# Optimization experiments

Hardware: AMD Instinct MI355X
Metric: run time of the kernel (lower is better)

## Reference

```python
import jax, jax.numpy as jnp
import numpy as np

R, B, N, H = 10, 8, 8192, 8          # ROIs, patients, nodes/ROI-graph, inner hidden
K = N // 2                            # TopKPooling ratio=0.5 -> ceil(0.5*N)
EPAIR = 65536                         # undirected edge pairs per patient graph
E = 2 * B * EPAIR                     # directed edges per ROI (both directions, all patients)
FIN = 4
HEADS, OH = 4, 16
SUPER_DIM = 2 * H + 3                 # (inner_layers+1)*hidden + 3 centroid coords = 19
EPS = 1e-5


def setup_inputs() -> dict:
    key = jax.random.key(0)
    ks = jax.random.split(key, 24)
    roi_x = jax.random.normal(ks[0], (R, B * N, FIN), jnp.float32)
    # within-graph undirected random edges, offset per patient
    u = jax.random.randint(ks[1], (R, B, EPAIR), 0, N)
    v = jax.random.randint(ks[2], (R, B, EPAIR), 0, N)
    off = (jnp.arange(B) * N)[None, :, None]
    src = jnp.concatenate([u + off, v + off], axis=-1).reshape(R, -1)
    dst = jnp.concatenate([v + off, u + off], axis=-1).reshape(R, -1)
    roi_edge_index = jnp.stack([src, dst], axis=1).astype(jnp.int32)  # [R, 2, E]
    centroids = jax.random.uniform(ks[3], (R, B, 3), jnp.float32) + 0.1  # nonzero -> all ROIs kept
    g = lambda k, s: jax.random.normal(k, s, jnp.float32) * 0.1
    return {
        'roi_x': roi_x,
        'roi_edge_index': roi_edge_index,
        'centroids': centroids,
        'gcn_w': g(ks[4], (R, FIN, H)),
        'gcn_b': g(ks[5], (R, H)),
        'ln_w': jnp.ones((R, H), jnp.float32),
        'ln_b': jnp.zeros((R, H), jnp.float32),
        'topk_w': g(ks[6], (R, H)),
        'gat1_w': g(ks[7], (SUPER_DIM, HEADS * OH)),
        'att_src1': g(ks[8], (HEADS, OH)),
        'att_dst1': g(ks[9], (HEADS, OH)),
        'gat1_b': g(ks[10], (HEADS * OH,)),
        'ln_o1_w': jnp.ones((HEADS * OH,), jnp.float32),
        'ln_o1_b': jnp.zeros((HEADS * OH,), jnp.float32),
        'gat2_w': g(ks[11], (HEADS * OH, OH)),
        'att_src2': g(ks[12], (1, OH)),
        'att_dst2': g(ks[13], (1, OH)),
        'gat2_b': g(ks[14], (OH,)),
        'ln_o2_w': jnp.ones((OH,), jnp.float32),
        'ln_o2_b': jnp.zeros((OH,), jnp.float32),
        'lin_w': g(ks[15], (OH, 2)),
        'lin_b': g(ks[16], (2,)),
    }


def _inner_roi(x, edges, cen, Wg, bg, wln, bln, wtk):
    """GCNConv(4,H)+ReLU -> graph-mode LayerNorm -> TopKPooling -> mean pools. x: [B*N, 4]."""
    src, dst = edges[0], edges[1]
    h = x @ Wg                                                     # [BN, H]
    # GCN symmetric norm with self loops: deg = in-degree + 1
    deg = jax.ops.segment_sum(jnp.ones((E,), x.dtype), dst, num_segments=B * N) + 1.0
    dis = deg ** -0.5
    norm = dis[src] * dis[dst]
    agg = jax.ops.segment_sum(h[src] * norm[:, None], dst, num_segments=B * N)
    h = jax.nn.relu(agg + h / deg[:, None] + bg)
    # PyG LayerNorm (mode='graph'): normalize over all nodes & channels per patient graph
    hb = h.reshape(B, N, H)
    mu = hb.mean(axis=(1, 2), keepdims=True)
    var = ((hb - mu) ** 2).mean(axis=(1, 2), keepdims=True)
    hn = (hb - mu) / jnp.sqrt(var + EPS) * wln + bln               # [B, N, H]
    res = hn.mean(axis=1)                                          # residual global_mean_pool [B, H]
    # TopKPooling: score = tanh(x.w/||w||); keep top K per graph; scale kept nodes by score
    s = jnp.tanh(jnp.einsum('bnh,h->bn', hn, wtk) / jnp.linalg.norm(wtk))
    vals, idx = jax.lax.top_k(s, K)                                # [B, K]
    sel = jnp.take_along_axis(hn, idx[:, :, None], axis=1) * vals[:, :, None]
    fv = sel.mean(axis=1)                                          # global_mean_pool after pooling
    return jnp.concatenate([res, fv, cen], axis=1)                 # [B, 19]


def _gat(x, src, dst, W, a_s, a_d, b, heads, oc):
    """PyG GATConv (self loops already included in src/dst)."""
    n = x.shape[0]
    h = (x @ W).reshape(n, heads, oc)
    es = (h * a_s).sum(-1)                                         # [n, heads]
    ed = (h * a_d).sum(-1)
    e = jax.nn.leaky_relu(es[src] + ed[dst], 0.2)                  # [E, heads]
    m = jax.ops.segment_max(e, dst, num_segments=n)
    ex = jnp.exp(e - m[dst])
    den = jax.ops.segment_sum(ex, dst, num_segments=n)
    alpha = ex / den[dst]
    out = jax.ops.segment_sum(h[src] * alpha[:, :, None], dst, num_segments=n)
    return out.reshape(n, heads * oc) + b


def _graph_ln(x, w, b):
    xb = x.reshape(B, R, -1)
    mu = xb.mean(axis=(1, 2), keepdims=True)
    var = ((xb - mu) ** 2).mean(axis=(1, 2), keepdims=True)
    return ((xb - mu) / jnp.sqrt(var + EPS) * w + b).reshape(B * R, -1)


def reference(roi_x, roi_edge_index, centroids, gcn_w, gcn_b, ln_w, ln_b, topk_w,
              gat1_w, att_src1, att_dst1, gat1_b, ln_o1_w, ln_o1_b,
              gat2_w, att_src2, att_dst2, gat2_b, ln_o2_w, ln_o2_b, lin_w, lin_b):
    feats = jax.vmap(_inner_roi)(roi_x, roi_edge_index, centroids,
                                 gcn_w, gcn_b, ln_w, ln_b, topk_w)   # [R, B, 19]
    super_x = feats.transpose(1, 0, 2).reshape(B * R, SUPER_DIM)      # patient-major node order
    # star edges 0->1..9 per patient, plus GATConv's default self loops
    pat = jnp.arange(B) * R
    sl = jnp.arange(B * R)
    ssrc = jnp.concatenate([jnp.repeat(pat, R - 1), sl])
    sdst = jnp.concatenate([(pat[:, None] + jnp.arange(1, R)).reshape(-1), sl])
    x1 = jax.nn.elu(_gat(super_x, ssrc, sdst, gat1_w, att_src1, att_dst1, gat1_b, HEADS, OH))
    x1 = _graph_ln(x1, ln_o1_w, ln_o1_b)
    x2 = jax.nn.elu(_gat(x1, ssrc, sdst, gat2_w, att_src2, att_dst2, gat2_b, 1, OH))
    x2 = _graph_ln(x2, ln_o2_w, ln_o2_b)
    pooled = x2.reshape(B, R, OH).mean(axis=1)                        # global_mean_pool
    # dropout p=0.5 is a no-op in eval mode
    return pooled @ lin_w + lin_b                                     # [B, 2]
```

## Files before the change

kernel.cpp:

```cpp
#include <hip/hip_runtime.h>
#include <hip/hip_bf16.h>
#include <math.h>

#define RR 10
#define BB 8
#define NN 8192
#define HH 8
#define BN 65536
#define EE (1u << 20)
#define EPB (EE / BB)
#define NPAIR (EPB / 2)
#define KK 4096
#define NSUP 80
#define CSRL4 34816

#define NTL(p) __builtin_nontemporal_load(p)
typedef int vi4 __attribute__((ext_vector_type(4)));

__global__ __launch_bounds__(1024)
void count_kernel(const int* __restrict__ ei, const float* __restrict__ x,
                  unsigned char* __restrict__ rankg,
                  unsigned short* __restrict__ qo8g, int* __restrict__ et8g,
                  float* __restrict__ zg) {
  const int bid = blockIdx.x;
  const int rb = bid % 80;
  const int p = bid / 80;
  const int r = rb / BB;
  const int b = rb % BB;
  const int tid = threadIdx.x;

  __shared__ int scnt[1024];
  __shared__ int ps[1024];
  scnt[tid] = 0;
  __syncthreads();

  const int* up = ei + (size_t)r * 2u * EE + (size_t)b * EPB;
  const int* vp = ei + (size_t)r * 2u * EE + EE + (size_t)b * EPB;
  unsigned char* rk = rankg + (size_t)rb * EPB;

#define CNT(U, V, E)                                                \
  {                                                                 \
    int lv = (V) & (NN - 1);                                        \
    if ((lv >> 10) == p) {                                          \
      int t0 = atomicAdd(&scnt[lv & 1023], 1);                      \
      rk[E] = (unsigned char)t0;                                    \
    }                                                               \
    int lu = (U) & (NN - 1);                                        \
    if ((lu >> 10) == p) {                                          \
      int t1 = atomicAdd(&scnt[lu & 1023], 1);                      \
      rk[(E) + NPAIR] = (unsigned char)t1;                          \
    }                                                               \
  }
#pragma unroll 4
  for (int it = 0; it < 16; ++it) {
    int e = it * 4096 + tid * 4;
    vi4 uu = NTL((const vi4*)(up + e));
    vi4 vv = NTL((const vi4*)(vp + e));
    CNT(uu.x, vv.x, e) CNT(uu.y, vv.y, e + 1)
    CNT(uu.z, vv.z, e + 2) CNT(uu.w, vv.w, e + 3)
  }
#undef CNT
  __syncthreads();

  int a = scnt[tid];
  ps[tid] = a;
  __syncthreads();
  for (int s2 = 1; s2 < 1024; s2 <<= 1) {
    int v = 0;
    if (tid >= s2) v = ps[tid - s2];
    __syncthreads();
    ps[tid] += v;
    __syncthreads();
  }
  int incl = ps[tid];
  qo8g[(size_t)rb * 8192 + (size_t)p * 1024 + tid] = (unsigned short)(incl - a);
  if (tid == 1023) et8g[rb * 8 + p] = incl;

  {
    int n = p * 1024 + tid;
    const float4* x4 = (const float4*)x + (size_t)r * BN + (size_t)b * NN;
    float4* z4 = (float4*)zg + (size_t)rb * NN;
    float ds = rsqrtf((float)a + 1.0f);
    float4 xv = x4[n];
    z4[n] = make_float4(xv.x * ds, xv.y * ds, xv.z * ds, xv.w * ds);
  }
}

__global__ __launch_bounds__(1024)
void scatfuse_kernel(const int* __restrict__ ei, const float* __restrict__ zg,
                     const unsigned char* __restrict__ rankg,
                     const unsigned short* __restrict__ qo8g, const int* __restrict__ et8g,
                     const float* __restrict__ gcn_w, const float* __restrict__ gcn_b,
                     const float* __restrict__ ln_w, const float* __restrict__ topk_w,
                     float* __restrict__ v4g, float* __restrict__ tg,
                     double* __restrict__ partsS, float* __restrict__ partsC) {
  const int bid = blockIdx.x;
  const int rb = bid % 80;
  const int q = bid / 80;
  const int r = rb / BB;
  const int b = rb % BB;
  const int tid = threadIdx.x;

  __shared__ unsigned short qoQ[2049];
  __shared__ __align__(16) unsigned short csrL[CSRL4];
  __shared__ int etq[2];

  if (tid < 2) etq[tid] = et8g[rb * 8 + q * 2 + tid];
  __syncthreads();
  const unsigned short* qo8 = qo8g + (size_t)rb * 8192 + (size_t)q * 2048;
  for (int i = tid; i < 2048; i += 1024)
    qoQ[i] = (unsigned short)((int)qo8[i] + ((i >= 1024) ? etq[0] : 0));
  if (tid == 0) qoQ[2048] = (unsigned short)(etq[0] + etq[1]);
  __syncthreads();

  const int* up = ei + (size_t)r * 2u * EE + (size_t)b * EPB;
  const int* vp = ei + (size_t)r * 2u * EE + EE + (size_t)b * EPB;
  const unsigned char* rk = rankg + (size_t)rb * EPB;

#define SCAT(U, V, RA, RB2)                                         \
  {                                                                 \
    int lv = (V) & (NN - 1);                                        \
    if ((lv >> 11) == q) {                                          \
      csrL[(int)qoQ[lv & 2047] + (int)(RA)] =                       \
          (unsigned short)((U) & (NN - 1));                         \
    }                                                               \
    int lu = (U) & (NN - 1);                                        \
    if ((lu >> 11) == q) {                                          \
      csrL[(int)qoQ[lu & 2047] + (int)(RB2)] =                      \
          (unsigned short)((V) & (NN - 1));                         \
    }                                                               \
  }
#pragma unroll 4
  for (int it = 0; it < 16; ++it) {
    int e = it * 4096 + tid * 4;
    unsigned ra = NTL((const unsigned*)(rk + e));
    unsigned rbv = NTL((const unsigned*)(rk + NPAIR + e));
    vi4 uu = NTL((const vi4*)(up + e));
    vi4 vv = NTL((const vi4*)(vp + e));
    SCAT(uu.x, vv.x, ra & 255u, rbv & 255u)
    SCAT(uu.y, vv.y, (ra >> 8) & 255u, (rbv >> 8) & 255u)
    SCAT(uu.z, vv.z, (ra >> 16) & 255u, (rbv >> 16) & 255u)
    SCAT(uu.w, vv.w, (ra >> 24) & 255u, (rbv >> 24) & 255u)
  }
#undef SCAT
  __syncthreads();

  const float* wp = gcn_w + r * 32;
  const float* bgp = gcn_b + r * 8;
  float lwwt[8];
#pragma unroll
  for (int c = 0; c < 8; ++c) lwwt[c] = ln_w[r * 8 + c] * topk_w[r * 8 + c];

  const float4* z4 = (const float4*)zg + (size_t)rb * NN;
  float4* v4o = (float4*)v4g + (size_t)rb * NN;
  float* trow = tg + (size_t)rb * NN;

  double s1 = 0.0, s2 = 0.0;
  float ch[8] = {0, 0, 0, 0, 0, 0, 0, 0};

#pragma unroll
  for (int k = 0; k < 2; ++k) {
    int idx = tid + k * 1024;
    int n = q * 2048 + idx;
    int o = (int)qoQ[idx];
    int c = (int)qoQ[idx + 1] - o;
    float4 zn = z4[n];
    float sx = zn.x, sy = zn.y, sz = zn.z, sw = zn.w;
    int j = 0;
    for (; j + 3 < c; j += 4) {
      int n0 = csrL[o + j], n1 = csrL[o + j + 1], n2 = csrL[o + j + 2], n3 = csrL[o + j + 3];
      float4 a0 = z4[n0], a1 = z4[n1], a2 = z4[n2], a3 = z4[n3];
      sx += a0.x + a1.x + a2.x + a3.x;
      sy += a0.y + a1.y + a2.y + a3.y;
      sz += a0.z + a1.z + a2.z + a3.z;
      sw += a0.w + a1.w + a2.w + a3.w;
    }
    for (; j < c; ++j) {
      int n0 = csrL[o + j];
      float4 a0 = z4[n0];
      sx += a0.x; sy += a0.y; sz += a0.z; sw += a0.w;
    }
    float dd = rsqrtf((float)c + 1.0f);
    float v0 = sx * dd, v1 = sy * dd, v2 = sz * dd, v3 = sw * dd;
    v4o[n] = make_float4(v0, v1, v2, v3);
    float t = 0.f;
#pragma unroll
    for (int cc = 0; cc < 8; ++cc) {
      float h = fmaxf(v0 * wp[cc] + v1 * wp[8 + cc] + v2 * wp[16 + cc] + v3 * wp[24 + cc] + bgp[cc], 0.0f);
      s1 += h;
      s2 += (double)h * h;
      ch[cc] += h;
      t += h * lwwt[cc];
    }
    trow[n] = t;
  }

  __syncthreads();
  double* wredS = (double*)csrL;
  float* wredC = (float*)(csrL + 512);
  int lane = tid & 63, wid = tid >> 6;
#pragma unroll
  for (int off = 32; off > 0; off >>= 1) {
    s1 += __shfl_down(s1, off);
    s2 += __shfl_down(s2, off);
#pragma unroll
    for (int cc = 0; cc < 8; ++cc) ch[cc] += __shfl_down(ch[cc], off);
  }
  if (lane == 0) {
    wredS[wid * 2] = s1;
    wredS[wid * 2 + 1] = s2;
#pragma unroll
    for (int cc = 0; cc < 8; ++cc) wredC[wid * 8 + cc] = ch[cc];
  }
  __syncthreads();
  if (tid == 0) {
    double a = 0.0, b3 = 0.0;
    for (int w2 = 0; w2 < 16; ++w2) { a += wredS[w2 * 2]; b3 += wredS[w2 * 2 + 1]; }
    partsS[bid * 2] = a;
    partsS[bid * 2 + 1] = b3;
  }
  if (tid < 8) {
    float sc = 0.f;
    for (int w2 = 0; w2 < 16; ++w2) sc += wredC[w2 * 8 + tid];
    partsC[bid * 8 + tid] = sc;
  }
}

__global__ __launch_bounds__(1024)
void roiB_kernel(const float* __restrict__ tg, const float* __restrict__ v4g,
                 const double* __restrict__ partsS, const float* __restrict__ partsC,
                 const float* __restrict__ gcn_w, const float* __restrict__ gcn_b,
                 const float* __restrict__ ln_w, const float* __restrict__ ln_b,
                 const float* __restrict__ topk_w, const float* __restrict__ cen,
                 float* __restrict__ feats) {
  const int rb = blockIdx.x;
  const int r = rb / BB;
  const int tid = threadIdx.x;
  const int lane = tid & 63, wid = tid >> 6;

  __shared__ int histW[16 * 256];
  __shared__ int wtot[16];
  __shared__ float chS[8];
  __shared__ float fvSum[8];
  __shared__ int cntGt;
  __shared__ int selb, kleft;
  __shared__ float sstat[2];

  float lw[8], lb[8], wt[8], w[32], bg[8];
  float wn2 = 0.f, L1 = 0.f, B1 = 0.f;
#pragma unroll
  for (int i = 0; i < 32; ++i) w[i] = gcn_w[r * 32 + i];
#pragma unroll
  for (int c = 0; c < 8; ++c) {
    lw[c] = ln_w[r * 8 + c];
    lb[c] = ln_b[r * 8 + c];
    wt[c] = topk_w[r * 8 + c];
    bg[c] = gcn_b[r * 8 + c];
    wn2 += wt[c] * wt[c];
    L1 += lw[c] * wt[c];
    B1 += lb[c] * wt[c];
  }
  const float invn = 1.0f / sqrtf(wn2);

  if (tid == 0) {
    double s1 = 0.0, s2 = 0.0;
    for (int q = 0; q < 4; ++q) {
      s1 += partsS[(q * 80 + rb) * 2];
      s2 += partsS[(q * 80 + rb) * 2 + 1];
    }
    const double M = (double)NN * HH;
    double mu = s1 / M;
    double var = s2 / M - mu * mu;
    sstat[0] = (float)mu;
    sstat[1] = (float)(1.0 / sqrt(var + 1e-5));
    cntGt = 0;
  }
  if (tid < 8) {
    float sc = 0.f;
    for (int q = 0; q < 4; ++q) sc += partsC[(q * 80 + rb) * 8 + tid];
    chS[tid] = sc;
    fvSum[tid] = 0.f;
  }
  __syncthreads();
  const float muf = sstat[0];
  const float rstd = sstat[1];
  const float C0 = B1 - rstd * muf * L1;

  const float* trow = tg + (size_t)rb * NN;
  float sv[8];
  unsigned fl[8];
#pragma unroll
  for (int i = 0; i < 8; ++i) {
    int n = tid * 8 + i;
    float s = tanhf((rstd * trow[n] + C0) * invn);
    sv[i] = s;
    unsigned u = __float_as_uint(s);
    fl[i] = (u & 0x80000000u) ? ~u : (u | 0x80000000u);
  }

  unsigned prefix = 0;
  int kneed = KK;
  for (int shift = 24; shift >= 0; shift -= 8) {
#pragma unroll
    for (int z = 0; z < 4; ++z) histW[tid + z * 1024] = 0;
    __syncthreads();
#pragma unroll
    for (int i = 0; i < 8; ++i) {
      bool m = (shift == 24) || ((fl[i] >> (shift + 8)) == prefix);
      if (m) atomicAdd(&histW[wid * 256 + ((fl[i] >> shift) & 255)], 1);
    }
    __syncthreads();
    if (wid == 0) {
      int b0 = lane * 4;
      int t0 = 0, t1 = 0, t2 = 0, t3 = 0;
      for (int w2 = 0; w2 < 16; ++w2) {
        const int* hp2 = &histW[w2 * 256 + b0];
        t0 += hp2[0]; t1 += hp2[1]; t2 += hp2[2]; t3 += hp2[3];
      }
      int s3 = t3, s2i = t2 + s3, s1i = t1 + s2i, s0 = t0 + s1i;
      int v = s0;
#pragma unroll
      for (int off = 1; off < 64; off <<= 1) {
        int o = __shfl_down(v, off);
        v += (lane + off < 64) ? o : 0;
      }
      int above = v - s0;
      int S3 = above + s3, S2 = above + s2i, S1 = above + s1i, S0 = above + s0;
      if (S3 >= kneed && above < kneed)      { selb = b0 + 3; kleft = kneed - above; }
      else if (S2 >= kneed && S3 < kneed)    { selb = b0 + 2; kleft = kneed - S3; }
      else if (S1 >= kneed && S2 < kneed)    { selb = b0 + 1; kleft = kneed - S2; }
      else if (S0 >= kneed && S1 < kneed)    { selb = b0;     kleft = kneed - S1; }
    }
    __syncthreads();
    prefix = (prefix << 8) | (unsigned)selb;
    kneed = kleft;
  }
  float tau = (prefix & 0x80000000u) ? __uint_as_float(prefix & 0x7fffffffu)
                                     : __uint_as_float(~prefix);

  int cg = 0, ct = 0;
#pragma unroll
  for (int i = 0; i < 8; ++i) {
    if (sv[i] > tau) cg++;
    else if (sv[i] == tau) ct++;
  }
  int wcg = cg;
#pragma unroll
  for (int off = 32; off > 0; off >>= 1) wcg += __shfl_down(wcg, off);
  if (lane == 0) atomicAdd(&cntGt, wcg);
  int sc = ct;
#pragma unroll
  for (int off = 1; off < 64; off <<= 1) {
    int o = __shfl_up(sc, off);
    if (lane >= off) sc += o;
  }
  if (lane == 63) wtot[wid] = sc;
  __syncthreads();
  int wbase = 0;
  for (int w2 = 0; w2 < wid; ++w2) wbase += wtot[w2];
  int rank = wbase + sc - ct;
  int quota = KK - cntGt;

  const float4* v4r = (const float4*)v4g + (size_t)rb * NN;
  float fva[8] = {0, 0, 0, 0, 0, 0, 0, 0};
#pragma unroll
  for (int i = 0; i < 8; ++i) {
    bool inc = sv[i] > tau;
    if (!inc && sv[i] == tau) { inc = (rank < quota); rank++; }
    if (inc) {
      int n = tid * 8 + i;
      float4 vv = v4r[n];
#pragma unroll
      for (int c = 0; c < 8; ++c) {
        float h = fmaxf(vv.x * w[c] + vv.y * w[8 + c] + vv.z * w[16 + c] + vv.w * w[24 + c] + bg[c], 0.0f);
        float hn = (h - muf) * rstd * lw[c] + lb[c];
        fva[c] += hn * sv[i];
      }
    }
  }
#pragma unroll
  for (int c = 0; c < 8; ++c) atomicAdd(&fvSum[c], fva[c]);
  __syncthreads();

  size_t fo = (size_t)rb * 19;
  if (tid < 8) {
    feats[fo + tid] = ((chS[tid] - (float)NN * muf) * rstd * lw[tid]) / (float)NN + lb[tid];
    feats[fo + 8 + tid] = fvSum[tid] / (float)KK;
  }
  if (tid >= 16 && tid < 19) {
    feats[fo + tid] = cen[(size_t)rb * 3 + (tid - 16)];
  }
}

__global__ __launch_bounds__(256)
void super_kernel(const float* __restrict__ feats,
                  const float* __restrict__ W1, const float* __restrict__ as1,
                  const float* __restrict__ ad1, const float* __restrict__ b1,
                  const float* __restrict__ lnw1, const float* __restrict__ lnb1,
                  const float* __restrict__ W2, const float* __restrict__ as2,
                  const float* __restrict__ ad2, const float* __restrict__ b2,
                  const float* __restrict__ lnw2, const float* __restrict__ lnb2,
                  const float* __restrict__ linw, const float* __restrict__ linb,
                  float* __restrict__ out) {
  __shared__ float sx[NSUP * 19];
  __shared__ float h1[NSUP * 64];
  __shared__ float x1[NSUP * 64];
  __shared__ float es1[NSUP * 4], ed1[NSUP * 4];
  __shared__ float h2[NSUP * 16], x2[NSUP * 16];
  __shared__ float es2[NSUP], ed2[NSUP];
  __shared__ float stat[16];
  const int tid = threadIdx.x;

  for (int i = tid; i < NSUP * 19; i += 256) {
    int n = i / 19, c = i % 19;
    int bb = n / RR, rr = n % RR;
    sx[i] = feats[(size_t)(rr * BB + bb) * 19 + c];
  }
  __syncthreads();
  for (int p = tid; p < NSUP * 64; p += 256) {
    int n = p / 64, j = p % 64;
    float acc = 0.f;
    for (int k2 = 0; k2 < 19; ++k2) acc += sx[n * 19 + k2] * W1[k2 * 64 + j];
    h1[p] = acc;
  }
  __syncthreads();
  for (int p = tid; p < NSUP * 4; p += 256) {
    int n = p / 4, hd = p % 4;
    float a = 0.f, d2 = 0.f;
    for (int o = 0; o < 16; ++o) {
      float hv = h1[n * 64 + hd * 16 + o];
      a += hv * as1[hd * 16 + o];
      d2 += hv * ad1[hd * 16 + o];
    }
    es1[p] = a; ed1[p] = d2;
  }
  __syncthreads();
  for (int p = tid; p < NSUP * 64; p += 256) {
    int n = p / 64, j = p % 64, hd = j / 16;
    int rr = n % RR;
    float o;
    if (rr == 0) {
      o = h1[p];
    } else {
      int hub = n - rr;
      float eh = es1[hub * 4 + hd] + ed1[n * 4 + hd];
      float esf = es1[n * 4 + hd] + ed1[n * 4 + hd];
      eh = eh > 0.f ? eh : 0.2f * eh;
      esf = esf > 0.f ? esf : 0.2f * esf;
      float m = fmaxf(eh, esf);
      float wh = expf(eh - m), ws2 = expf(esf - m);
      o = (wh * h1[hub * 64 + j] + ws2 * h1[n * 64 + j]) / (wh + ws2);
    }
    float v = o + b1[j];
    x1[p] = v > 0.f ? v : expm1f(v);
  }
  __syncthreads();
  if (tid < BB) {
    double m = 0.0, v2 = 0.0;
    for (int q = 0; q < RR * 64; ++q) {
      float val = x1[tid * RR * 64 + q];
      m += val; v2 += (double)val * val;
    }
    m /= (RR * 64.0); v2 = v2 / (RR * 64.0) - m * m;
    stat[tid] = (float)m;
    stat[8 + tid] = (float)(1.0 / sqrt(v2 + 1e-5));
  }
  __syncthreads();
  for (int p = tid; p < NSUP * 64; p += 256) {
    int n = p / 64, j = p % 64, bb = n / RR;
    x1[p] = (x1[p] - stat[bb]) * stat[8 + bb] * lnw1[j] + lnb1[j];
  }
  __syncthreads();
  for (int p = tid; p < NSUP * 16; p += 256) {
    int n = p / 16, o = p % 16;
    float acc = 0.f;
    for (int j = 0; j < 64; ++j) acc += x1[n * 64 + j] * W2[j * 16 + o];
    h2[p] = acc;
  }
  __syncthreads();
  for (int n = tid; n < NSUP; n += 256) {
    float a = 0.f, d2 = 0.f;
    for (int o = 0; o < 16; ++o) {
      float hv = h2[n * 16 + o];
      a += hv * as2[o];
      d2 += hv * ad2[o];
    }
    es2[n] = a; ed2[n] = d2;
  }
  __syncthreads();
  for (int p = tid; p < NSUP * 16; p += 256) {
    int n = p / 16, o = p % 16;
    int rr = n % RR;
    float ov;
    if (rr == 0) ov = h2[p];
    else {
      int hub = n - rr;
      float eh = es2[hub] + ed2[n];
      float esf = es2[n] + ed2[n];
      eh = eh > 0.f ? eh : 0.2f * eh;
      esf = esf > 0.f ? esf : 0.2f * esf;
      float m = fmaxf(eh, esf);
      float wh = expf(eh - m), ws2 = expf(esf - m);
      ov = (wh * h2[hub * 16 + o] + ws2 * h2[p]) / (wh + ws2);
    }
    float v = ov + b2[o];
    x2[p] = v > 0.f ? v : expm1f(v);
  }
  __syncthreads();
  if (tid < BB) {
    double m = 0.0, v2 = 0.0;
    for (int q = 0; q < RR * 16; ++q) {
      float val = x2[tid * RR * 16 + q];
      m += val; v2 += (double)val * val;
    }
    m /= (RR * 16.0); v2 = v2 / (RR * 16.0) - m * m;
    stat[tid] = (float)m;
    stat[8 + tid] = (float)(1.0 / sqrt(v2 + 1e-5));
  }
  __syncthreads();
  for (int p = tid; p < NSUP * 16; p += 256) {
    int n = p / 16, o = p % 16, bb = n / RR;
    x2[p] = (x2[p] - stat[bb]) * stat[8 + bb] * lnw2[o] + lnb2[o];
  }
  __syncthreads();
  if (tid < BB * 2) {
    int bb = tid / 2, t = tid % 2;
    float acc = linb[t];
    for (int o = 0; o < 16; ++o) {
      float pm = 0.f;
      for (int rr = 0; rr < RR; ++rr) pm += x2[(bb * RR + rr) * 16 + o];
      pm /= (float)RR;
      acc += pm * linw[o * 2 + t];
    }
    out[bb * 2 + t] = acc;
  }
}

extern "C" void kernel_launch(void* const* d_in, const int* in_sizes, int n_in,
                              void* d_out, int out_size, void* d_ws, size_t ws_size,
                              hipStream_t stream) {
  const float* roi_x = (const float*)d_in[0];
  const int* ei = (const int*)d_in[1];
  const float* cen = (const float*)d_in[2];
  const float* gcn_w = (const float*)d_in[3];
  const float* gcn_b = (const float*)d_in[4];
  const float* ln_w = (const float*)d_in[5];
  const float* ln_b = (const float*)d_in[6];
  const float* topk_w = (const float*)d_in[7];
  const float* gat1_w = (const float*)d_in[8];
  const float* as1 = (const float*)d_in[9];
  const float* ad1 = (const float*)d_in[10];
  const float* b1 = (const float*)d_in[11];
  const float* lnw1 = (const float*)d_in[12];
  const float* lnb1 = (const float*)d_in[13];
  const float* W2 = (const float*)d_in[14];
  const float* as2 = (const float*)d_in[15];
  const float* ad2 = (const float*)d_in[16];
  const float* b2 = (const float*)d_in[17];
  const float* lnw2 = (const float*)d_in[18];
  const float* lnb2 = (const float*)d_in[19];
  const float* linw = (const float*)d_in[20];
  const float* linb = (const float*)d_in[21];
  float* out = (float*)d_out;

  char* wsb = (char*)d_ws;
  float* v4g = (float*)wsb;
  float* zg = (float*)(wsb + (size_t)80 * NN * 4 * 4);
  float* tg = (float*)((char*)zg + (size_t)80 * NN * 4 * 4);
  double* partsS = (double*)((char*)tg + (size_t)80 * NN * 4);
  float* partsC = (float*)((char*)partsS + 640 * 8);
  unsigned short* qo8 = (unsigned short*)((char*)partsC + 2560 * 4);
  int* et8 = (int*)((char*)qo8 + (size_t)80 * 8192 * 2);
  float* feats = (float*)((char*)et8 + 640 * 4);
  unsigned char* rankg = (unsigned char*)((char*)feats + (size_t)RR * BB * 19 * 4);

  count_kernel<<<640, 1024, 0, stream>>>(ei, roi_x, rankg, qo8, et8, zg);
  scatfuse_kernel<<<320, 1024, 0, stream>>>(ei, zg, rankg, qo8, et8,
                                            gcn_w, gcn_b, ln_w, topk_w,
                                            v4g, tg, partsS, partsC);
  roiB_kernel<<<80, 1024, 0, stream>>>(tg, v4g, partsS, partsC,
                                       gcn_w, gcn_b, ln_w, ln_b, topk_w, cen, feats);
  super_kernel<<<1, 256, 0, stream>>>(feats, gat1_w, as1, ad1, b1, lnw1, lnb1,
                                      W2, as2, ad2, b2, lnw2, lnb2, linw, linb, out);
}
```

Baseline: 221.3 us.

## Split scatter-fuse into eighth-graph blocks of 512 threads

The scatter/aggregate kernel now has each block own 1024 destination nodes (one eighth of a graph) instead of 2048, launching 640 blocks of 512 threads rather than 320 of 1024. The per-block CSR shared buffer halves, so more blocks can be resident per CU and the GPU is more evenly filled. The cost is that every block still streams the full edge list of its graph, so global edge reads double, and the downstream partial reductions now sum 8 parts instead of 4.

New measurement: 217.8 us. About the same (-1.6%).

```diff
diff --git a/kernel.cpp b/kernel.cpp
--- a/kernel.cpp
+++ b/kernel.cpp
@@ -12,7 +12,7 @@
 #define NPAIR (EPB / 2)
 #define KK 4096
 #define NSUP 80
-#define CSRL4 34816
+#define CSRL8 17408
 
 #define NTL(p) __builtin_nontemporal_load(p)
 typedef int vi4 __attribute__((ext_vector_type(4)));
@@ -86,7 +86,7 @@
   }
 }
 
-__global__ __launch_bounds__(1024)
+__global__ __launch_bounds__(512)
 void scatfuse_kernel(const int* __restrict__ ei, const float* __restrict__ zg,
                      const unsigned char* __restrict__ rankg,
                      const unsigned short* __restrict__ qo8g, const int* __restrict__ et8g,
@@ -96,21 +96,17 @@
                      double* __restrict__ partsS, float* __restrict__ partsC) {
   const int bid = blockIdx.x;
   const int rb = bid % 80;
-  const int q = bid / 80;
+  const int e8 = bid / 80;
   const int r = rb / BB;
   const int b = rb % BB;
   const int tid = threadIdx.x;
 
-  __shared__ unsigned short qoQ[2049];
-  __shared__ __align__(16) unsigned short csrL[CSRL4];
-  __shared__ int etq[2];
-
-  if (tid < 2) etq[tid] = et8g[rb * 8 + q * 2 + tid];
-  __syncthreads();
-  const unsigned short* qo8 = qo8g + (size_t)rb * 8192 + (size_t)q * 2048;
-  for (int i = tid; i < 2048; i += 1024)
-    qoQ[i] = (unsigned short)((int)qo8[i] + ((i >= 1024) ? etq[0] : 0));
-  if (tid == 0) qoQ[2048] = (unsigned short)(etq[0] + etq[1]);
+  __shared__ unsigned short qoE[1025];
+  __shared__ __align__(16) unsigned short csrL[CSRL8];
+
+  const unsigned short* qo8 = qo8g + (size_t)rb * 8192 + (size_t)e8 * 1024;
+  for (int i = tid; i < 1024; i += 512) qoE[i] = qo8[i];
+  if (tid == 0) qoE[1024] = (unsigned short)et8g[rb * 8 + e8];
   __syncthreads();
 
   const int* up = ei + (size_t)r * 2u * EE + (size_t)b * EPB;
@@ -120,19 +116,19 @@
 #define SCAT(U, V, RA, RB2)                                         \
   {                                                                 \
     int lv = (V) & (NN - 1);                                        \
-    if ((lv >> 11) == q) {                                          \
-      csrL[(int)qoQ[lv & 2047] + (int)(RA)] =                       \
+    if ((lv >> 10) == e8) {                                         \
+      csrL[(int)qoE[lv & 1023] + (int)(RA)] =                       \
           (unsigned short)((U) & (NN - 1));                         \
     }                                                               \
     int lu = (U) & (NN - 1);                                        \
-    if ((lu >> 11) == q) {                                          \
-      csrL[(int)qoQ[lu & 2047] + (int)(RB2)] =                      \
+    if ((lu >> 10) == e8) {                                         \
+      csrL[(int)qoE[lu & 1023] + (int)(RB2)] =                      \
           (unsigned short)((V) & (NN - 1));                         \
     }                                                               \
   }
 #pragma unroll 4
-  for (int it = 0; it < 16; ++it) {
-    int e = it * 4096 + tid * 4;
+  for (int it = 0; it < 32; ++it) {
+    int e = it * 2048 + tid * 4;
     unsigned ra = NTL((const unsigned*)(rk + e));
     unsigned rbv = NTL((const unsigned*)(rk + NPAIR + e));
     vi4 uu = NTL((const vi4*)(up + e));
@@ -160,10 +156,10 @@
 
 #pragma unroll
   for (int k = 0; k < 2; ++k) {
-    int idx = tid + k * 1024;
-    int n = q * 2048 + idx;
-    int o = (int)qoQ[idx];
-    int c = (int)qoQ[idx + 1] - o;
+    int idx = tid + k * 512;
+    int n = e8 * 1024 + idx;
+    int o = (int)qoE[idx];
+    int c = (int)qoE[idx + 1] - o;
     float4 zn = z4[n];
     float sx = zn.x, sy = zn.y, sz = zn.z, sw = zn.w;
     int j = 0;
@@ -215,13 +211,13 @@
   __syncthreads();
   if (tid == 0) {
     double a = 0.0, b3 = 0.0;
-    for (int w2 = 0; w2 < 16; ++w2) { a += wredS[w2 * 2]; b3 += wredS[w2 * 2 + 1]; }
+    for (int w2 = 0; w2 < 8; ++w2) { a += wredS[w2 * 2]; b3 += wredS[w2 * 2 + 1]; }
     partsS[bid * 2] = a;
     partsS[bid * 2 + 1] = b3;
   }
   if (tid < 8) {
     float sc = 0.f;
-    for (int w2 = 0; w2 < 16; ++w2) sc += wredC[w2 * 8 + tid];
+    for (int w2 = 0; w2 < 8; ++w2) sc += wredC[w2 * 8 + tid];
     partsC[bid * 8 + tid] = sc;
   }
 }
@@ -264,9 +260,9 @@
 
   if (tid == 0) {
     double s1 = 0.0, s2 = 0.0;
-    for (int q = 0; q < 4; ++q) {
-      s1 += partsS[(q * 80 + rb) * 2];
-      s2 += partsS[(q * 80 + rb) * 2 + 1];
+    for (int p = 0; p < 8; ++p) {
+      s1 += partsS[(p * 80 + rb) * 2];
+      s2 += partsS[(p * 80 + rb) * 2 + 1];
     }
     const double M = (double)NN * HH;
     double mu = s1 / M;
@@ -277,7 +273,7 @@
   }
   if (tid < 8) {
     float sc = 0.f;
-    for (int q = 0; q < 4; ++q) sc += partsC[(q * 80 + rb) * 8 + tid];
+    for (int p = 0; p < 8; ++p) sc += partsC[(p * 80 + rb) * 8 + tid];
     chS[tid] = sc;
     fvSum[tid] = 0.f;
   }
@@ -568,16 +564,16 @@
   float* zg = (float*)(wsb + (size_t)80 * NN * 4 * 4);
   float* tg = (float*)((char*)zg + (size_t)80 * NN * 4 * 4);
   double* partsS = (double*)((char*)tg + (size_t)80 * NN * 4);
-  float* partsC = (float*)((char*)partsS + 640 * 8);
-  unsigned short* qo8 = (unsigned short*)((char*)partsC + 2560 * 4);
+  float* partsC = (float*)((char*)partsS + 1280 * 8);
+  unsigned short* qo8 = (unsigned short*)((char*)partsC + 5120 * 4);
   int* et8 = (int*)((char*)qo8 + (size_t)80 * 8192 * 2);
   float* feats = (float*)((char*)et8 + 640 * 4);
   unsigned char* rankg = (unsigned char*)((char*)feats + (size_t)RR * BB * 19 * 4);
 
   count_kernel<<<640, 1024, 0, stream>>>(ei, roi_x, rankg, qo8, et8, zg);
-  scatfuse_kernel<<<320, 1024, 0, stream>>>(ei, zg, rankg, qo8, et8,
-                                            gcn_w, gcn_b, ln_w, topk_w,
-                                            v4g, tg, partsS, partsC);
+  scatfuse_kernel<<<640, 512, 0, stream>>>(ei, zg, rankg, qo8, et8,
+                                           gcn_w, gcn_b, ln_w, topk_w,
+                                           v4g, tg, partsS, partsC);
   roiB_kernel<<<80, 1024, 0, stream>>>(tg, v4g, partsS, partsC,
                                        gcn_w, gcn_b, ln_w, ln_b, topk_w, cen, feats);
   super_kernel<<<1, 256, 0, stream>>>(feats, gat1_w, as1, ad1, b1, lnw1, lnb1,
```
